# Kernel tuning notes

Measured on AMD Instinct MI355X. Metric: run time of the kernel, lower is better.

## Reference

```python
import jax, jax.numpy as jnp
import numpy as np

# config mirroring init_kwargs
PPD = (64, 64)                      # points_per_dim (spatial grid)
GRID_RANGE = ((-1.0, 1.0), (-1.0, 1.0))
B, N, NT, DX, DZ = 2, 2048, 8, 3, 16
INIT_LS = 0.1
TIME_DIM = 0


def construct_grid():
    axes = [jnp.linspace(lo, hi, p, dtype=jnp.float32) for (lo, hi), p in zip(GRID_RANGE, PPD)]
    mesh = jnp.meshgrid(*axes, indexing='ij')
    return jnp.stack(mesh, axis=-1)  # (H, W, 2)


def setup_inputs() -> dict:
    key = jax.random.key(0)
    k1, k2, k3 = jax.random.split(key, 3)
    x = jax.random.uniform(k1, (B, N, DX), jnp.float32, -1.0, 1.0)
    z = jax.random.normal(k2, (B, N, DZ), jnp.float32)
    time_grid = jnp.sort(jax.random.uniform(k3, (B, NT), jnp.float32, -1.0, 1.0), axis=-1)
    # raw parameter s.t. softplus(param) == INIT_LS (inverse-softplus init)
    lengthscale_param = jnp.full((DX,), float(np.log(np.exp(INIT_LS) - 1.0)), jnp.float32)
    return {"x": x, "z": z, "time_grid": time_grid, "lengthscale_param": lengthscale_param}


def reference(x, z, time_grid, lengthscale_param):
    H, W = PPD
    b = x.shape[0]
    t = time_grid.shape[1]
    grid = construct_grid()  # (H, W, 2)

    ls = 1e-5 + jax.nn.softplus(lengthscale_param)  # (DX,)

    # x_grid: [b, t, H, W, DX] with the time coordinate at coord index TIME_DIM(=0)
    spatial = jnp.broadcast_to(grid, (b, t, H, W, 2))
    tg = jnp.broadcast_to(time_grid[:, :, None, None, None], (b, t, H, W, 1))
    x_grid = jnp.concatenate([tg, spatial], axis=-1)

    G = t * H * W
    xg_flat = x_grid.reshape(b, G, DX)

    # pre_exp[b, g, n] = sum_d (xg - x)^2 / ls_d^2, computed via scaled-coordinate
    # norm expansion to avoid materializing the [b, G, n, DX] difference tensor.
    a = xg_flat / ls                          # [b, G, DX]
    c = x / ls                                # [b, n, DX]
    pre_exp = (jnp.sum(a * a, axis=-1)[:, :, None]
               + jnp.sum(c * c, axis=-1)[:, None, :]
               - 2.0 * jnp.einsum('bgd,bnd->bgn', a, c))
    weights = jnp.exp(-0.5 * pre_exp)         # [b, G, n]  (RBF weights)

    z_grid = jnp.einsum('bgn,bne->bge', weights, z)  # [b, G, DZ]
    z_grid = z_grid.reshape(b, t, H, W, DZ)
    return x_grid, z_grid
```

## Files before the change

### kernel.cpp

```cpp
#include <hip/hip_runtime.h>
#include <math.h>

#define B_  2
#define N_  2048
#define NT_ 8
#define DZ_ 16
#define H_  64
#define W_  64

#define XGRID_SIZE (B_*NT_*H_*W_*3)
#define CUT 12.0f
#define CH  128

using half8   = __attribute__((ext_vector_type(8))) _Float16;
using floatx4 = __attribute__((ext_vector_type(4))) float;

#if __has_builtin(__builtin_amdgcn_exp2f)
#define EXP2(xx) __builtin_amdgcn_exp2f(xx)
#else
#define EXP2(xx) exp2f(xx)
#endif

__global__ __launch_bounds__(256, 4) void fused_kernel(
    const float* __restrict__ x,
    const float* __restrict__ z,
    const float* __restrict__ tg,
    const float* __restrict__ lsp,
    float* __restrict__ out)
{
    const int i    = blockIdx.x & 63;
    const int t    = (blockIdx.x >> 6) & 7;
    const int b    = blockIdx.x >> 9;
    const int tid  = threadIdx.x;
    const int w    = tid >> 6;
    const int lane = tid & 63;
    const int quad = lane >> 4;
    const int col  = lane & 15;

    const float step = 2.0f / 63.0f;
    const float C    = 0.84932180f;

    const float r0 = C / (1e-5f + log1pf(expf(lsp[0])));
    const float r1 = C / (1e-5f + log1pf(expf(lsp[1])));
    const float r2 = C / (1e-5f + log1pf(expf(lsp[2])));

    const float tval = tg[b*NT_ + t];
    const float gi   = -1.0f + step * (float)i;

    union REDU {
        float2 cuc[N_ + CH];
        float  red[4][64][DZ_ + 1];
    };
    __shared__ REDU sm;
    __shared__ int  cidx[N_ + CH];
    __shared__ int  wsum[4];

    const float* __restrict__ xb = x + b*N_*3;
    float sq[8], cx[8];
    int keepm = 0;
    {
        const float4* __restrict__ xb4 = (const float4*)xb;
        float f[24];
        #pragma unroll
        for (int q = 0; q < 6; ++q) {
            float4 v = xb4[tid*6 + q];
            f[q*4+0] = v.x; f[q*4+1] = v.y; f[q*4+2] = v.z; f[q*4+3] = v.w;
        }
        #pragma unroll
        for (int r = 0; r < 8; ++r) {
            float dt = (tval - f[3*r+0]) * r0;
            float di = (gi   - f[3*r+1]) * r1;
            sq[r] = fmaf(dt, dt, di*di);
            cx[r] = f[3*r+2] * r2;
            if (sq[r] < CUT) keepm |= (1 << r);
        }
    }
    const int cnt = __popc(keepm);
    const unsigned long long below = (1ull << lane) - 1ull;
    int pre = 0, wtot = 0;
    #pragma unroll
    for (int bit = 0; bit < 4; ++bit) {
        unsigned long long bb = __ballot((cnt >> bit) & 1);
        pre  += __popcll(bb & below) << bit;
        wtot += __popcll(bb) << bit;
    }
    if (lane == 0) wsum[w] = wtot;
    __syncthreads();

    int woff = 0, M = 0;
    #pragma unroll
    for (int ww = 0; ww < 4; ++ww) {
        int s = wsum[ww];
        woff += (ww < w) ? s : 0;
        M    += s;
    }
    {
        int pos = woff + pre;
        #pragma unroll
        for (int r = 0; r < 8; ++r) {
            if ((keepm >> r) & 1) {
                sm.cuc[pos] = make_float2(sq[r], cx[r]);
                cidx[pos]   = tid*8 + r;
                ++pos;
            }
        }
    }
    if (tid < CH) {
        sm.cuc[M + tid] = make_float2(1e9f, 0.f);
        cidx[M + tid]   = 0;
    }

    if (tid < 192) {
        int jj = tid / 3;
        int c  = tid - jj*3;
        float gj = -1.0f + step * (float)jj;
        float v  = (c == 0) ? tval : ((c == 1) ? gi : gj);
        out[(size_t)blockIdx.x * 192 + tid] = v;
    }
    __syncthreads();

    const int NC = (M + CH - 1) / CH;

    const float* __restrict__ zb = z + b*N_*DZ_;
    const int koff = w*32 + (quad << 3);

    const float aj0 = (-1.0f + step * (float)( 0 + col)) * r2;
    const float aj1 = (-1.0f + step * (float)(16 + col)) * r2;
    const float aj2 = (-1.0f + step * (float)(32 + col)) * r2;
    const float aj3 = (-1.0f + step * (float)(48 + col)) * r2;

    floatx4 acc0 = {0.f,0.f,0.f,0.f};
    floatx4 acc1 = {0.f,0.f,0.f,0.f};
    floatx4 acc2 = {0.f,0.f,0.f,0.f};
    floatx4 acc3 = {0.f,0.f,0.f,0.f};

    float zreg[8];
    {
        int idx[8];
        #pragma unroll
        for (int jj = 0; jj < 8; ++jj) idx[jj] = cidx[koff + jj];
        #pragma unroll
        for (int jj = 0; jj < 8; ++jj)
            zreg[jj] = zb[(size_t)idx[jj] * DZ_ + col];
    }

    for (int c = 0; c < NC; ++c) {
        half8 bf;
        #pragma unroll
        for (int jj = 0; jj < 8; ++jj) bf[jj] = (_Float16)zreg[jj];

        const int base = c*CH + koff;
        float2 mm[8];
        #pragma unroll
        for (int jj = 0; jj < 8; ++jj) mm[jj] = sm.cuc[base + jj];

        if (c + 1 < NC) {
            const int base2 = (c + 1)*CH + koff;
            int idx[8];
            #pragma unroll
            for (int jj = 0; jj < 8; ++jj) idx[jj] = cidx[base2 + jj];
            #pragma unroll
            for (int jj = 0; jj < 8; ++jj)
                zreg[jj] = zb[(size_t)idx[jj] * DZ_ + col];
        }

        half8 a0, a1, a2, a3;
        #pragma unroll
        for (int jj = 0; jj < 8; ++jj) {
            float s  = mm[jj].x;
            float cxv = mm[jj].y;
            float d0 = aj0 - cxv;
            float d1 = aj1 - cxv;
            float d2 = aj2 - cxv;
            float d3 = aj3 - cxv;
            a0[jj] = (_Float16)EXP2(-fmaf(d0, d0, s));
            a1[jj] = (_Float16)EXP2(-fmaf(d1, d1, s));
            a2[jj] = (_Float16)EXP2(-fmaf(d2, d2, s));
            a3[jj] = (_Float16)EXP2(-fmaf(d3, d3, s));
        }

        acc0 = __builtin_amdgcn_mfma_f32_16x16x32_f16(a0, bf, acc0, 0, 0, 0);
        acc1 = __builtin_amdgcn_mfma_f32_16x16x32_f16(a1, bf, acc1, 0, 0, 0);
        acc2 = __builtin_amdgcn_mfma_f32_16x16x32_f16(a2, bf, acc2, 0, 0, 0);
        acc3 = __builtin_amdgcn_mfma_f32_16x16x32_f16(a3, bf, acc3, 0, 0, 0);
    }

    __syncthreads();

    #pragma unroll
    for (int r = 0; r < 4; ++r) sm.red[w][ 0 + quad*4 + r][col] = acc0[r];
    #pragma unroll
    for (int r = 0; r < 4; ++r) sm.red[w][16 + quad*4 + r][col] = acc1[r];
    #pragma unroll
    for (int r = 0; r < 4; ++r) sm.red[w][32 + quad*4 + r][col] = acc2[r];
    #pragma unroll
    for (int r = 0; r < 4; ++r) sm.red[w][48 + quad*4 + r][col] = acc3[r];
    __syncthreads();

    const int jj = tid >> 2;
    const int eg = (tid & 3) * 4;
    float4 s4 = make_float4(0.f, 0.f, 0.f, 0.f);
    #pragma unroll
    for (int ww = 0; ww < 4; ++ww) {
        s4.x += sm.red[ww][jj][eg + 0];
        s4.y += sm.red[ww][jj][eg + 1];
        s4.z += sm.red[ww][jj][eg + 2];
        s4.w += sm.red[ww][jj][eg + 3];
    }
    float* og = out + XGRID_SIZE + (size_t)blockIdx.x * (W_ * DZ_);
    *(float4*)(og + jj*DZ_ + eg) = s4;
}

extern "C" void kernel_launch(void* const* d_in, const int* in_sizes, int n_in,
                              void* d_out, int out_size, void* d_ws, size_t ws_size,
                              hipStream_t stream) {
    const float* x   = (const float*)d_in[0];
    const float* z   = (const float*)d_in[1];
    const float* tg  = (const float*)d_in[2];
    const float* lsp = (const float*)d_in[3];

    float* out = (float*)d_out;

    fused_kernel<<<1024, 256, 0, stream>>>(x, z, tg, lsp, out);
}
```

Baseline: 69.55 us.

## Split each grid row across two blocks and pack point index into distance bits

Each block now handles half of a W row (32 columns) instead of all 64, doubling the grid to 2048 blocks. The point index is packed into the low 11 mantissa bits of the stored squared distance, which removes the separate cidx shared array and cuts LDS use. Launch bounds are raised to 6 blocks per CU for more occupancy. In exchange, the per-point x loading, culling, compaction and z gathers are now done twice per row, and the distance value loses a little precision.

```diff
diff --git a/kernel.cpp b/kernel.cpp
--- a/kernel.cpp
+++ b/kernel.cpp
@@ -21,16 +21,18 @@
 #define EXP2(xx) exp2f(xx)
 #endif
 
-__global__ __launch_bounds__(256, 4) void fused_kernel(
+__global__ __launch_bounds__(256, 6) void fused_kernel(
     const float* __restrict__ x,
     const float* __restrict__ z,
     const float* __restrict__ tg,
     const float* __restrict__ lsp,
     float* __restrict__ out)
 {
-    const int i    = blockIdx.x & 63;
-    const int t    = (blockIdx.x >> 6) & 7;
-    const int b    = blockIdx.x >> 9;
+    const int jh   = blockIdx.x & 1;
+    const int rid  = blockIdx.x >> 1;
+    const int i    = rid & 63;
+    const int t    = (rid >> 6) & 7;
+    const int b    = rid >> 9;
     const int tid  = threadIdx.x;
     const int w    = tid >> 6;
     const int lane = tid & 63;
@@ -49,10 +51,9 @@
 
     union REDU {
         float2 cuc[N_ + CH];
-        float  red[4][64][DZ_ + 1];
+        float  red[4][32][DZ_ + 1];
     };
     __shared__ REDU sm;
-    __shared__ int  cidx[N_ + CH];
     __shared__ int  wsum[4];
 
     const float* __restrict__ xb = x + b*N_*3;
@@ -99,23 +100,22 @@
         #pragma unroll
         for (int r = 0; r < 8; ++r) {
             if ((keepm >> r) & 1) {
-                sm.cuc[pos] = make_float2(sq[r], cx[r]);
-                cidx[pos]   = tid*8 + r;
+                unsigned int sb = (__float_as_uint(sq[r]) & ~2047u)
+                                | (unsigned int)(tid*8 + r);
+                sm.cuc[pos] = make_float2(__uint_as_float(sb), cx[r]);
                 ++pos;
             }
         }
     }
-    if (tid < CH) {
-        sm.cuc[M + tid] = make_float2(1e9f, 0.f);
-        cidx[M + tid]   = 0;
-    }
-
-    if (tid < 192) {
-        int jj = tid / 3;
-        int c  = tid - jj*3;
+    if (tid < CH) sm.cuc[M + tid] = make_float2(1e9f, 0.f);
+
+    if (tid < 96) {
+        int e  = jh*96 + tid;
+        int jj = e / 3;
+        int c  = e - jj*3;
         float gj = -1.0f + step * (float)jj;
         float v  = (c == 0) ? tval : ((c == 1) ? gi : gj);
-        out[(size_t)blockIdx.x * 192 + tid] = v;
+        out[(size_t)rid * 192 + e] = v;
     }
     __syncthreads();
 
@@ -124,24 +124,19 @@
     const float* __restrict__ zb = z + b*N_*DZ_;
     const int koff = w*32 + (quad << 3);
 
-    const float aj0 = (-1.0f + step * (float)( 0 + col)) * r2;
-    const float aj1 = (-1.0f + step * (float)(16 + col)) * r2;
-    const float aj2 = (-1.0f + step * (float)(32 + col)) * r2;
-    const float aj3 = (-1.0f + step * (float)(48 + col)) * r2;
+    const float ajA = (-1.0f + step * (float)(jh*32 +  0 + col)) * r2;
+    const float ajB = (-1.0f + step * (float)(jh*32 + 16 + col)) * r2;
 
     floatx4 acc0 = {0.f,0.f,0.f,0.f};
     floatx4 acc1 = {0.f,0.f,0.f,0.f};
-    floatx4 acc2 = {0.f,0.f,0.f,0.f};
-    floatx4 acc3 = {0.f,0.f,0.f,0.f};
 
     float zreg[8];
     {
-        int idx[8];
-        #pragma unroll
-        for (int jj = 0; jj < 8; ++jj) idx[jj] = cidx[koff + jj];
-        #pragma unroll
-        for (int jj = 0; jj < 8; ++jj)
-            zreg[jj] = zb[(size_t)idx[jj] * DZ_ + col];
+        #pragma unroll
+        for (int jj = 0; jj < 8; ++jj) {
+            unsigned int u = __float_as_uint(sm.cuc[koff + jj].x) & 2047u;
+            zreg[jj] = zb[(size_t)u * DZ_ + col];
+        }
     }
 
     for (int c = 0; c < NC; ++c) {
@@ -156,33 +151,26 @@
 
         if (c + 1 < NC) {
             const int base2 = (c + 1)*CH + koff;
-            int idx[8];
             #pragma unroll
-            for (int jj = 0; jj < 8; ++jj) idx[jj] = cidx[base2 + jj];
-            #pragma unroll
-            for (int jj = 0; jj < 8; ++jj)
-                zreg[jj] = zb[(size_t)idx[jj] * DZ_ + col];
-        }
-
-        half8 a0, a1, a2, a3;
+            for (int jj = 0; jj < 8; ++jj) {
+                unsigned int u = __float_as_uint(sm.cuc[base2 + jj].x) & 2047u;
+                zreg[jj] = zb[(size_t)u * DZ_ + col];
+            }
+        }
+
+        half8 a0, a1;
         #pragma unroll
         for (int jj = 0; jj < 8; ++jj) {
-            float s  = mm[jj].x;
+            float s   = mm[jj].x;
             float cxv = mm[jj].y;
-            float d0 = aj0 - cxv;
-            float d1 = aj1 - cxv;
-            float d2 = aj2 - cxv;
-            float d3 = aj3 - cxv;
+            float d0 = ajA - cxv;
+            float d1 = ajB - cxv;
             a0[jj] = (_Float16)EXP2(-fmaf(d0, d0, s));
             a1[jj] = (_Float16)EXP2(-fmaf(d1, d1, s));
-            a2[jj] = (_Float16)EXP2(-fmaf(d2, d2, s));
-            a3[jj] = (_Float16)EXP2(-fmaf(d3, d3, s));
         }
 
         acc0 = __builtin_amdgcn_mfma_f32_16x16x32_f16(a0, bf, acc0, 0, 0, 0);
         acc1 = __builtin_amdgcn_mfma_f32_16x16x32_f16(a1, bf, acc1, 0, 0, 0);
-        acc2 = __builtin_amdgcn_mfma_f32_16x16x32_f16(a2, bf, acc2, 0, 0, 0);
-        acc3 = __builtin_amdgcn_mfma_f32_16x16x32_f16(a3, bf, acc3, 0, 0, 0);
     }
 
     __syncthreads();
@@ -191,24 +179,22 @@
     for (int r = 0; r < 4; ++r) sm.red[w][ 0 + quad*4 + r][col] = acc0[r];
     #pragma unroll
     for (int r = 0; r < 4; ++r) sm.red[w][16 + quad*4 + r][col] = acc1[r];
-    #pragma unroll
-    for (int r = 0; r < 4; ++r) sm.red[w][32 + quad*4 + r][col] = acc2[r];
-    #pragma unroll
-    for (int r = 0; r < 4; ++r) sm.red[w][48 + quad*4 + r][col] = acc3[r];
-    __syncthreads();
-
-    const int jj = tid >> 2;
-    const int eg = (tid & 3) * 4;
-    float4 s4 = make_float4(0.f, 0.f, 0.f, 0.f);
-    #pragma unroll
-    for (int ww = 0; ww < 4; ++ww) {
-        s4.x += sm.red[ww][jj][eg + 0];
-        s4.y += sm.red[ww][jj][eg + 1];
-        s4.z += sm.red[ww][jj][eg + 2];
-        s4.w += sm.red[ww][jj][eg + 3];
-    }
-    float* og = out + XGRID_SIZE + (size_t)blockIdx.x * (W_ * DZ_);
-    *(float4*)(og + jj*DZ_ + eg) = s4;
+    __syncthreads();
+
+    if (tid < 128) {
+        const int jj = tid >> 2;
+        const int eg = (tid & 3) * 4;
+        float4 s4 = make_float4(0.f, 0.f, 0.f, 0.f);
+        #pragma unroll
+        for (int ww = 0; ww < 4; ++ww) {
+            s4.x += sm.red[ww][jj][eg + 0];
+            s4.y += sm.red[ww][jj][eg + 1];
+            s4.z += sm.red[ww][jj][eg + 2];
+            s4.w += sm.red[ww][jj][eg + 3];
+        }
+        float* og = out + XGRID_SIZE + (size_t)rid * (W_ * DZ_) + jh * (32 * DZ_);
+        *(float4*)(og + jj*DZ_ + eg) = s4;
+    }
 }
 
 extern "C" void kernel_launch(void* const* d_in, const int* in_sizes, int n_in,
@@ -221,5 +207,5 @@
 
     float* out = (float*)d_out;
 
-    fused_kernel<<<1024, 256, 0, stream>>>(x, z, tg, lsp, out);
+    fused_kernel<<<2048, 256, 0, stream>>>(x, z, tg, lsp, out);
 }
```

New measurement: 72.44 us. +4.1%, slower.

## Pack point index into squared-distance low bits, drop index LDS array, remap blocks

Applied to the files above, without the earlier changes.

Removes the separate shared-memory index array by storing each kept point's index in the low 11 mantissa bits of its partial squared distance. This cuts LDS use and the separate index loads, and launch bounds are raised to allow 5 blocks per CU. Block IDs are also remapped so that (b,t) vary fastest, which interleaves batches and times across concurrently running blocks to balance load. The cost is a small precision loss in the partial distance term that feeds the exponent.

```diff
diff --git a/kernel.cpp b/kernel.cpp
--- a/kernel.cpp
+++ b/kernel.cpp
@@ -21,16 +21,18 @@
 #define EXP2(xx) exp2f(xx)
 #endif
 
-__global__ __launch_bounds__(256, 4) void fused_kernel(
+__global__ __launch_bounds__(256, 5) void fused_kernel(
     const float* __restrict__ x,
     const float* __restrict__ z,
     const float* __restrict__ tg,
     const float* __restrict__ lsp,
     float* __restrict__ out)
 {
-    const int i    = blockIdx.x & 63;
-    const int t    = (blockIdx.x >> 6) & 7;
-    const int b    = blockIdx.x >> 9;
+    const int bid  = blockIdx.x;
+    const int i    = bid >> 4;
+    const int t    = (bid >> 1) & 7;
+    const int b    = bid & 1;
+    const int rid  = (b << 9) | (t << 6) | i;
     const int tid  = threadIdx.x;
     const int w    = tid >> 6;
     const int lane = tid & 63;
@@ -52,7 +54,6 @@
         float  red[4][64][DZ_ + 1];
     };
     __shared__ REDU sm;
-    __shared__ int  cidx[N_ + CH];
     __shared__ int  wsum[4];
 
     const float* __restrict__ xb = x + b*N_*3;
@@ -99,23 +100,21 @@
         #pragma unroll
         for (int r = 0; r < 8; ++r) {
             if ((keepm >> r) & 1) {
-                sm.cuc[pos] = make_float2(sq[r], cx[r]);
-                cidx[pos]   = tid*8 + r;
+                unsigned int sb = (__float_as_uint(sq[r]) & ~2047u)
+                                | (unsigned int)(tid*8 + r);
+                sm.cuc[pos] = make_float2(__uint_as_float(sb), cx[r]);
                 ++pos;
             }
         }
     }
-    if (tid < CH) {
-        sm.cuc[M + tid] = make_float2(1e9f, 0.f);
-        cidx[M + tid]   = 0;
-    }
+    if (tid < CH) sm.cuc[M + tid] = make_float2(1e9f, 0.f);
 
     if (tid < 192) {
         int jj = tid / 3;
         int c  = tid - jj*3;
         float gj = -1.0f + step * (float)jj;
         float v  = (c == 0) ? tval : ((c == 1) ? gi : gj);
-        out[(size_t)blockIdx.x * 192 + tid] = v;
+        out[(size_t)rid * 192 + tid] = v;
     }
     __syncthreads();
 
@@ -136,12 +135,11 @@
 
     float zreg[8];
     {
-        int idx[8];
-        #pragma unroll
-        for (int jj = 0; jj < 8; ++jj) idx[jj] = cidx[koff + jj];
-        #pragma unroll
-        for (int jj = 0; jj < 8; ++jj)
-            zreg[jj] = zb[(size_t)idx[jj] * DZ_ + col];
+        #pragma unroll
+        for (int jj = 0; jj < 8; ++jj) {
+            unsigned int u = __float_as_uint(sm.cuc[koff + jj].x) & 2047u;
+            zreg[jj] = zb[(size_t)u * DZ_ + col];
+        }
     }
 
     for (int c = 0; c < NC; ++c) {
@@ -156,18 +154,17 @@
 
         if (c + 1 < NC) {
             const int base2 = (c + 1)*CH + koff;
-            int idx[8];
             #pragma unroll
-            for (int jj = 0; jj < 8; ++jj) idx[jj] = cidx[base2 + jj];
-            #pragma unroll
-            for (int jj = 0; jj < 8; ++jj)
-                zreg[jj] = zb[(size_t)idx[jj] * DZ_ + col];
+            for (int jj = 0; jj < 8; ++jj) {
+                unsigned int u = __float_as_uint(sm.cuc[base2 + jj].x) & 2047u;
+                zreg[jj] = zb[(size_t)u * DZ_ + col];
+            }
         }
 
         half8 a0, a1, a2, a3;
         #pragma unroll
         for (int jj = 0; jj < 8; ++jj) {
-            float s  = mm[jj].x;
+            float s   = mm[jj].x;
             float cxv = mm[jj].y;
             float d0 = aj0 - cxv;
             float d1 = aj1 - cxv;
@@ -207,7 +204,7 @@
         s4.z += sm.red[ww][jj][eg + 2];
         s4.w += sm.red[ww][jj][eg + 3];
     }
-    float* og = out + XGRID_SIZE + (size_t)blockIdx.x * (W_ * DZ_);
+    float* og = out + XGRID_SIZE + (size_t)rid * (W_ * DZ_);
     *(float4*)(og + jj*DZ_ + eg) = s4;
 }
 
```

New measurement: 69.09 us. About the same (-0.7%).
